# Kernel optimization log

Hardware: AMD Instinct MI355X
Metric: run time of the kernel (lower is better)

Reference implementation:

```python
import jax, jax.numpy as jnp
import numpy as np

EMBED_DIM = 1024
NUM_HEADS = 16
HEAD_DIM = EMBED_DIM // NUM_HEADS


def setup_inputs() -> dict:
    key = jax.random.key(0)
    k1, k2, k3, k4 = jax.random.split(key, 4)
    B, S, D = 2, 2048, EMBED_DIM
    x = jax.random.normal(k1, (B, S, D), dtype=jnp.float32)
    xpos = jax.random.randint(k2, (B, S), 0, 2048, dtype=jnp.int32)
    # torch nn.Linear weights: [out_features, in_features]; qkv_bias=False -> no qkv bias
    qkv_w = jax.random.normal(k3, (3 * D, D), dtype=jnp.float32) * (D ** -0.5)
    proj_w = jax.random.normal(k4, (D, D), dtype=jnp.float32) * (D ** -0.5)
    proj_b = jnp.zeros((D,), dtype=jnp.float32)
    return {"x": x, "xpos": xpos, "qkv_w": qkv_w, "proj_w": proj_w, "proj_b": proj_b}


def reference(x, xpos, qkv_w, proj_w, proj_b):
    # rope is None, dropout rates are 0, so xpos is unused and dropout is identity.
    B, S, D = x.shape
    H, hd = NUM_HEADS, D // NUM_HEADS
    scale = hd ** -0.5

    qkv = x @ qkv_w.T                                   # [B, S, 3D]
    qkv = qkv.reshape(B, S, 3, H, hd)
    qkv = jnp.transpose(qkv, (0, 3, 2, 1, 4))           # [B, H, 3, S, hd]
    q, k, v = qkv[:, :, 0], qkv[:, :, 1], qkv[:, :, 2]  # each [B, H, S, hd]

    scores = jnp.einsum("bhqd,bhkd->bhqk", q, k) * scale  # [B, H, S, S]
    probs = jax.nn.softmax(scores, axis=-1)
    out = jnp.einsum("bhqk,bhkd->bhqd", probs, v)         # [B, H, S, hd]

    out = jnp.transpose(out, (0, 2, 1, 3)).reshape(B, S, D)
    out = out @ proj_w.T + proj_b
    return out
```

## Files before the change

kernel.cpp:

```cpp
#include <hip/hip_runtime.h>


typedef __bf16 bf16_8 __attribute__((ext_vector_type(8)));
typedef __bf16 bf16_4 __attribute__((ext_vector_type(4)));
typedef __bf16 bf16_2 __attribute__((ext_vector_type(2)));
typedef float floatx2 __attribute__((ext_vector_type(2)));
typedef float floatx4 __attribute__((ext_vector_type(4)));
typedef float floatx16 __attribute__((ext_vector_type(16)));
typedef unsigned uintx4 __attribute__((ext_vector_type(4)));

#define MFMA16 __builtin_amdgcn_mfma_f32_16x16x32_bf16
#define MFMA32 __builtin_amdgcn_mfma_f32_32x32x16_bf16
#define CSCALE 0.1803368801111204f
#define EXP2R  __builtin_amdgcn_exp2f

__device__ __forceinline__ void gld16(const __bf16* g, __bf16* l) {
    __builtin_amdgcn_global_load_lds(
        (const __attribute__((address_space(1))) void*)g,
        (__attribute__((address_space(3))) void*)l, 16, 0, 0);
}

__device__ __forceinline__ unsigned cvtpk_bf16(float a, float b) {
    unsigned d;
    __asm__("v_cvt_pk_bf16_f32 %0, %1, %2" : "=v"(d) : "v"(a), "v"(b));
    return d;
}

__device__ __forceinline__ void pl32swap(unsigned& a, unsigned& b) {
    __asm__ __volatile__("v_permlane32_swap_b32 %0, %1" : "+v"(a), "+v"(b));
}

__global__ __launch_bounds__(256) void cvt_all(
    const float* __restrict__ x, const float* __restrict__ w1,
    const float* __restrict__ w2,
    __bf16* __restrict__ xb, __bf16* __restrict__ w1b, __bf16* __restrict__ w2b)
{
    const int i = blockIdx.x * 256 + threadIdx.x;
    const float* src; __bf16* dst; int off;
    if (i < (1 << 20))                  { src = x;  dst = xb;  off = i; }
    else if (i < (1 << 20) + 786432)    { src = w1; dst = w1b; off = i - (1 << 20); }
    else                                { src = w2; dst = w2b; off = i - (1 << 20) - 786432; }
    float4 v = ((const float4*)src)[off];
    bf16_4 o;
    o[0] = (__bf16)v.x; o[1] = (__bf16)v.y; o[2] = (__bf16)v.z; o[3] = (__bf16)v.w;
    ((bf16_4*)dst)[off] = o;
}

__global__ __launch_bounds__(512) void qkv_gemm(
    const __bf16* __restrict__ X, const __bf16* __restrict__ W,
    __bf16* __restrict__ q_ws, __bf16* __restrict__ k_ws, __bf16* __restrict__ vt_ws)
{
    __shared__ __align__(16) __bf16 S[2][2][128 * 32];

    const int tid = threadIdx.x, lane = tid & 63, wv = tid >> 6;
    const int quad = lane >> 4, l15 = lane & 15;
    const int wm = (wv >> 2) * 64, wn = (wv & 3) * 32;
    const int m0 = blockIdx.y * 128, n0 = blockIdx.x * 128;
    const int c = n0 >> 10;

    const __bf16* Abase;
    const __bf16* Bbase;
    if (c == 2) { Abase = X + (size_t)m0 * 1024; Bbase = W + (size_t)n0 * 1024; }
    else        { Abase = W + (size_t)n0 * 1024; Bbase = X + (size_t)m0 * 1024; }

    const int srow = tid >> 2, skc = tid & 3;
    const int ssw  = ((skc ^ (srow & 3)) * 8);

#define QKV_STAGE(buf, k0)                                                     \
    {                                                                          \
        gld16(Abase + srow * 1024 + (k0) + ssw, &S[buf][0][tid * 8]);          \
        gld16(Bbase + srow * 1024 + (k0) + ssw, &S[buf][1][tid * 8]);          \
    }

    floatx4 acc[4][2] = {};
    QKV_STAGE(0, 0)
    __syncthreads();

#pragma unroll 1
    for (int kk = 0; kk < 32; ++kk) {
        const int cur = kk & 1;
        if (kk < 31) QKV_STAGE(cur ^ 1, (kk + 1) * 32)

        const __bf16* As = S[cur][0];
        const __bf16* Bs = S[cur][1];
        bf16_8 af[4], bf[2];
#pragma unroll
        for (int mt = 0; mt < 4; ++mt) {
            int r = wm + mt * 16 + l15;
            af[mt] = *(const bf16_8*)&As[r * 32 + ((quad ^ (r & 3)) * 8)];
        }
#pragma unroll
        for (int nt = 0; nt < 2; ++nt) {
            int r = wn + nt * 16 + l15;
            bf[nt] = *(const bf16_8*)&Bs[r * 32 + ((quad ^ (r & 3)) * 8)];
        }
#pragma unroll
        for (int mt = 0; mt < 4; ++mt)
#pragma unroll
            for (int nt = 0; nt < 2; ++nt)
                acc[mt][nt] = MFMA16(af[mt], bf[nt], acc[mt][nt], 0, 0, 0);

        if (kk < 31) {
            __asm__ __volatile__("s_waitcnt vmcnt(0)" ::: "memory");
            __syncthreads();
        }
    }

    if (c == 2) {
#pragma unroll
        for (int mt = 0; mt < 4; ++mt) {
            const int mbase = m0 + wm + mt * 16 + quad * 4;
            const int b = mbase >> 11, s = mbase & 2047;
#pragma unroll
            for (int nt = 0; nt < 2; ++nt) {
                const int n = n0 + wn + nt * 16 + l15;
                const int h = (n >> 6) & 15, d = n & 63;
                bf16_4 pk;
#pragma unroll
                for (int r = 0; r < 4; ++r) pk[r] = (__bf16)acc[mt][nt][r];
                *(bf16_4*)&vt_ws[((size_t)(b * 16 + h) * 64 + d) * 2048 + s] = pk;
            }
        }
    } else {
        __bf16* dst = (c == 0) ? q_ws : k_ws;
        const float scale = (c == 1) ? CSCALE : 1.0f;
#pragma unroll
        for (int mt = 0; mt < 4; ++mt) {
            const int nn = n0 + wm + mt * 16 + quad * 4;
            const int h = (nn >> 6) & 15, d0 = nn & 63;
#pragma unroll
            for (int nt = 0; nt < 2; ++nt) {
                const int token = m0 + wn + nt * 16 + l15;
                const int b = token >> 11, skey = token & 2047;
                bf16_4 pk;
#pragma unroll
                for (int r = 0; r < 4; ++r) pk[r] = (__bf16)(acc[mt][nt][r] * scale);
                *(bf16_4*)&dst[((size_t)(b * 16 + h) * 2048 + skey) * 64 + d0] = pk;
            }
        }
    }
#undef QKV_STAGE
}

__global__ __launch_bounds__(512, 4) void attn_kernel(
    const __bf16* __restrict__ q_ws, const __bf16* __restrict__ k_ws,
    const __bf16* __restrict__ vt_ws, __bf16* __restrict__ attn_ws)
{
    __shared__ __align__(16) __bf16 Ks [2][2][64 * 64];
    __shared__ __align__(16) __bf16 Vts[2][2][64 * 64];

    const int tid = threadIdx.x, lane = tid & 63, w = tid >> 6;
    const int l31 = lane & 31, hi = lane >> 5;
    const int qtile = w & 3, keyhalf = w >> 2;
    const int htid = tid & 255;

    const int linear = blockIdx.x + (blockIdx.y << 4);
    const int r = linear >> 3;
    const int bh = ((linear & 7) << 2) + (r & 3);
    const int qt = r >> 2;
    const int q0 = qt * 128 + qtile * 32;

    const __bf16* __restrict__ qp  = q_ws  + (size_t)bh * (2048 * 64);
    const __bf16* __restrict__ kp  = k_ws  + (size_t)bh * (2048 * 64);
    const __bf16* __restrict__ vtp = vt_ws + (size_t)bh * (64 * 2048);
    const int koff = keyhalf * 1024;

    const int srow = htid >> 3, skc = htid & 7;
    const int sw   = (skc ^ (srow & 7)) * 8;
    const __bf16* kb0 = kp  + (size_t)(koff + srow) * 64 + sw;
    const __bf16* kb1 = kp  + (size_t)(koff + srow + 32) * 64 + sw;
    const __bf16* vb0 = vtp + (size_t)srow * 2048 + koff + sw;
    const __bf16* vb1 = vtp + (size_t)(srow + 32) * 2048 + koff + sw;
    const int ldsoff = htid * 8;

    bf16_8 qf[4];
    {
        const int qrow = q0 + l31;
#pragma unroll
        for (int s = 0; s < 4; ++s)
            qf[s] = *(const bf16_8*)&qp[qrow * 64 + s * 16 + hi * 8];
    }

    floatx16 oacc[2] = {};
    floatx2 ls2[4] = {};
    const floatx16 fzero = {};

    gld16(kb0, &Ks [keyhalf][0][ldsoff]);
    gld16(kb1, &Ks [keyhalf][0][ldsoff + 2048]);
    gld16(vb0, &Vts[keyhalf][0][ldsoff]);
    gld16(vb1, &Vts[keyhalf][0][ldsoff + 2048]);
    __syncthreads();

#pragma unroll 1
    for (int kt = 0; kt < 16; ++kt) {
        const int cur = kt & 1;
        if (kt < 15) {
            const int ko = (kt + 1) * 64;
            gld16(kb0 + ko * 64, &Ks [keyhalf][cur ^ 1][ldsoff]);
            gld16(kb1 + ko * 64, &Ks [keyhalf][cur ^ 1][ldsoff + 2048]);
            gld16(vb0 + ko,      &Vts[keyhalf][cur ^ 1][ldsoff]);
            gld16(vb1 + ko,      &Vts[keyhalf][cur ^ 1][ldsoff + 2048]);
        }
        const __bf16* Kb = Ks [keyhalf][cur];
        const __bf16* Vb = Vts[keyhalf][cur];

        floatx16 sacc[2];
        __builtin_amdgcn_s_setprio(1);
        {
            const int kc0 = hi;
            const int r0 = l31, r1 = 32 + l31;
            bf16_8 kf0 = *(const bf16_8*)&Kb[r0 * 64 + ((kc0 ^ (r0 & 7)) * 8)];
            bf16_8 kf1 = *(const bf16_8*)&Kb[r1 * 64 + ((kc0 ^ (r1 & 7)) * 8)];
            sacc[0] = MFMA32(kf0, qf[0], fzero, 0, 0, 0);
            sacc[1] = MFMA32(kf1, qf[0], fzero, 0, 0, 0);
        }
#pragma unroll
        for (int s = 1; s < 4; ++s) {
            const int kc = s * 2 + hi;
#pragma unroll
            for (int t = 0; t < 2; ++t) {
                const int row = t * 32 + l31;
                bf16_8 kf = *(const bf16_8*)&Kb[row * 64 + ((kc ^ (row & 7)) * 8)];
                sacc[t] = MFMA32(kf, qf[s], sacc[t], 0, 0, 0);
            }
        }
        __builtin_amdgcn_s_setprio(0);

#pragma unroll
        for (int s = 0; s < 4; ++s) {
            const int t = s >> 1, b2 = (s & 1) * 2;
            unsigned Dw[4];
#pragma unroll
            for (int jr = 0; jr < 2; ++jr)
#pragma unroll
                for (int e = 0; e < 2; ++e) {
                    const int j = b2 + jr;
                    float pa = EXP2R(sacc[t][j * 4 + e * 2]);
                    float pb = EXP2R(sacc[t][j * 4 + e * 2 + 1]);
                    floatx2 p2; p2[0] = pa; p2[1] = pb;
                    ls2[t * 2 + e] += p2;
                    Dw[jr * 2 + e] = cvtpk_bf16(pa, pb);
                }
            unsigned x0 = Dw[0], y0 = Dw[2];
            unsigned x1 = Dw[1], y1 = Dw[3];
            pl32swap(x0, y0);
            pl32swap(x1, y1);
            uintx4 uu; uu[0] = x0; uu[1] = x1; uu[2] = y0; uu[3] = y1;
            const bf16_8 pf = __builtin_bit_cast(bf16_8, uu);
            const int kc = s * 2 + hi;
            __builtin_amdgcn_s_setprio(1);
#pragma unroll
            for (int dt = 0; dt < 2; ++dt) {
                const int drow = dt * 32 + l31;
                bf16_8 vf = *(const bf16_8*)&Vb[drow * 64 + ((kc ^ (drow & 7)) * 8)];
                oacc[dt] = MFMA32(vf, pf, oacc[dt], 0, 0, 0);
            }
            __builtin_amdgcn_s_setprio(0);
        }

        if (kt < 15) {
            __asm__ __volatile__("s_waitcnt vmcnt(0)" ::: "memory");
            __syncthreads();
        }
    }

    const floatx2 lv = (ls2[0] + ls2[1]) + (ls2[2] + ls2[3]);
    const float lsum = lv[0] + lv[1];
    const float lw = lsum + __shfl_xor(lsum, 32, 64);

    __syncthreads();
    floatx4* comb  = (floatx4*)&Ks[0][0][0];
    float*   lcomb = (float*)&Vts[0][0][0];

    if (keyhalf == 1) {
#pragma unroll
        for (int dt = 0; dt < 2; ++dt)
#pragma unroll
            for (int g = 0; g < 4; ++g) {
                floatx4 v4;
#pragma unroll
                for (int r4 = 0; r4 < 4; ++r4) v4[r4] = oacc[dt][g * 4 + r4];
                comb[((qtile * 8 + dt * 4 + g) << 6) + lane] = v4;
            }
        lcomb[(qtile << 6) + lane] = lw;
    }
    __syncthreads();
    if (keyhalf == 0) {
        const int b = bh >> 4, h = bh & 15;
        const float inv_l = 1.0f / (lw + lcomb[(qtile << 6) + lane]);
        const int token = b * 2048 + q0 + l31;
#pragma unroll
        for (int dt = 0; dt < 2; ++dt)
#pragma unroll
            for (int g = 0; g < 4; ++g) {
                const floatx4 v2 = comb[((qtile * 8 + dt * 4 + g) << 6) + lane];
                bf16_4 ok;
#pragma unroll
                for (int r4 = 0; r4 < 4; ++r4)
                    ok[r4] = (__bf16)((oacc[dt][g * 4 + r4] + v2[r4]) * inv_l);
                *(bf16_4*)&attn_ws[(size_t)token * 1024 + h * 64 + dt * 32 + g * 8 + hi * 4] = ok;
            }
    }
}

__device__ __forceinline__ void proj_stage(
    const __bf16* __restrict__ A, const __bf16* __restrict__ Bp,
    int k0, __bf16* As, __bf16* Bs, int tid)
{
    const int srow = tid >> 3, skc = tid & 7;
    const int ssw  = (skc ^ (srow & 7)) * 8;
#pragma unroll
    for (int it = 0; it < 2; ++it) {
        const int row = srow + it * 64;
        gld16(A + row * 1024 + k0 + ssw, &As[(it * 512 + tid) * 8]);
    }
    gld16(Bp + srow * 1024 + k0 + ssw, &Bs[tid * 8]);
}

__global__ __launch_bounds__(512) void proj_gemm(
    const __bf16* __restrict__ Ain, const __bf16* __restrict__ W,
    const float* __restrict__ bias, float* __restrict__ out)
{
    __shared__ __align__(16) __bf16 As[2][128 * 64];
    __shared__ __align__(16) __bf16 Bs[2][64 * 64];
    floatx4 acc[2][2] = {};
    const int m0 = blockIdx.y * 128, n0 = blockIdx.x * 64;

    const int tid = threadIdx.x, lane = tid & 63, wv = tid >> 6;
    const int quad = lane >> 4, l15 = lane & 15;
    const int wm = (wv >> 1) * 32, wn = (wv & 1) * 32;

    const __bf16* A  = Ain + (size_t)m0 * 1024;
    const __bf16* Bp = W   + (size_t)n0 * 1024;

    proj_stage(A, Bp, 0, As[0], Bs[0], tid);
    __syncthreads();

#pragma unroll 1
    for (int kk = 0; kk < 16; ++kk) {
        const int cur = kk & 1;
        if (kk < 15)
            proj_stage(A, Bp, (kk + 1) * 64, As[cur ^ 1], Bs[cur ^ 1], tid);

        const __bf16* Ab = As[cur];
        const __bf16* Bb = Bs[cur];
#pragma unroll
        for (int ks = 0; ks < 2; ++ks) {
            bf16_8 af[2], bf[2];
#pragma unroll
            for (int mt = 0; mt < 2; ++mt) {
                int r = wm + mt * 16 + l15;
                af[mt] = *(const bf16_8*)&Ab[r * 64 + (((ks * 4 + quad) ^ (r & 7)) * 8)];
            }
#pragma unroll
            for (int nt = 0; nt < 2; ++nt) {
                int r = wn + nt * 16 + l15;
                bf[nt] = *(const bf16_8*)&Bb[r * 64 + (((ks * 4 + quad) ^ (r & 7)) * 8)];
            }
#pragma unroll
            for (int mt = 0; mt < 2; ++mt)
#pragma unroll
                for (int nt = 0; nt < 2; ++nt)
                    acc[mt][nt] = MFMA16(af[mt], bf[nt], acc[mt][nt], 0, 0, 0);
        }

        if (kk < 15) {
            __asm__ __volatile__("s_waitcnt vmcnt(0)" ::: "memory");
            __syncthreads();
        }
    }

    float bv[2];
#pragma unroll
    for (int nt = 0; nt < 2; ++nt) bv[nt] = bias[n0 + wn + nt * 16 + l15];

#pragma unroll
    for (int mt = 0; mt < 2; ++mt) {
        const int m = m0 + wm + mt * 16 + quad * 4;
#pragma unroll
        for (int nt = 0; nt < 2; ++nt) {
            const int n = n0 + wn + nt * 16 + l15;
#pragma unroll
            for (int r = 0; r < 4; ++r)
                out[(size_t)(m + r) * 1024 + n] = acc[mt][nt][r] + bv[nt];
        }
    }
}

extern "C" void kernel_launch(void* const* d_in, const int* in_sizes, int n_in,
                              void* d_out, int out_size, void* d_ws, size_t ws_size,
                              hipStream_t stream)
{
    const float* x      = (const float*)d_in[0];
    const float* qkv_w  = (const float*)d_in[2];
    const float* proj_w = (const float*)d_in[3];
    const float* proj_b = (const float*)d_in[4];
    float* out = (float*)d_out;

    const size_t SZ   = 4096 * 1024;
    const size_t WQKV = 3072 * 1024;
    const size_t WPRJ = 1024 * 1024;

    __bf16* xb      = (__bf16*)d_ws;
    __bf16* qkvwb   = xb + SZ;
    __bf16* projwb  = qkvwb + WQKV;
    __bf16* q_ws    = projwb + WPRJ;
    __bf16* k_ws    = q_ws + SZ;
    __bf16* vt_ws   = k_ws + SZ;
    __bf16* attn_ws = vt_ws + SZ;

    cvt_all<<<dim3(8192), 256, 0, stream>>>(x, qkv_w, proj_w, xb, qkvwb, projwb);
    qkv_gemm  <<<dim3(24, 32), 512, 0, stream>>>(xb, qkvwb, q_ws, k_ws, vt_ws);
    attn_kernel<<<dim3(16, 32), 512, 0, stream>>>(q_ws, k_ws, vt_ws, attn_ws);
    proj_gemm <<<dim3(16, 32), 512, 0, stream>>>(attn_ws, projwb, proj_b, out);
}
```

Measured before the change: 176.2 us.

## Fuse fp32-to-bf16 conversion into QKV and projection GEMM loaders

Measured after the change: 178.6 us. No clear change (+1.3%).

```diff
diff --git a/kernel.cpp b/kernel.cpp
--- a/kernel.cpp
+++ b/kernel.cpp
@@ -20,6 +20,13 @@
         (__attribute__((address_space(3))) void*)l, 16, 0, 0);
 }
 
+__device__ __forceinline__ bf16_8 cvt8(float4 a, float4 b) {
+    bf16_8 o;
+    o[0] = (__bf16)a.x; o[1] = (__bf16)a.y; o[2] = (__bf16)a.z; o[3] = (__bf16)a.w;
+    o[4] = (__bf16)b.x; o[5] = (__bf16)b.y; o[6] = (__bf16)b.z; o[7] = (__bf16)b.w;
+    return o;
+}
+
 __device__ __forceinline__ unsigned cvtpk_bf16(float a, float b) {
     unsigned d;
     __asm__("v_cvt_pk_bf16_f32 %0, %1, %2" : "=v"(d) : "v"(a), "v"(b));
@@ -30,24 +37,8 @@
     __asm__ __volatile__("v_permlane32_swap_b32 %0, %1" : "+v"(a), "+v"(b));
 }
 
-__global__ __launch_bounds__(256) void cvt_all(
-    const float* __restrict__ x, const float* __restrict__ w1,
-    const float* __restrict__ w2,
-    __bf16* __restrict__ xb, __bf16* __restrict__ w1b, __bf16* __restrict__ w2b)
-{
-    const int i = blockIdx.x * 256 + threadIdx.x;
-    const float* src; __bf16* dst; int off;
-    if (i < (1 << 20))                  { src = x;  dst = xb;  off = i; }
-    else if (i < (1 << 20) + 786432)    { src = w1; dst = w1b; off = i - (1 << 20); }
-    else                                { src = w2; dst = w2b; off = i - (1 << 20) - 786432; }
-    float4 v = ((const float4*)src)[off];
-    bf16_4 o;
-    o[0] = (__bf16)v.x; o[1] = (__bf16)v.y; o[2] = (__bf16)v.z; o[3] = (__bf16)v.w;
-    ((bf16_4*)dst)[off] = o;
-}
-
 __global__ __launch_bounds__(512) void qkv_gemm(
-    const __bf16* __restrict__ X, const __bf16* __restrict__ W,
+    const float* __restrict__ X, const float* __restrict__ W,
     __bf16* __restrict__ q_ws, __bf16* __restrict__ k_ws, __bf16* __restrict__ vt_ws)
 {
     __shared__ __align__(16) __bf16 S[2][2][128 * 32];
@@ -58,28 +49,37 @@
     const int m0 = blockIdx.y * 128, n0 = blockIdx.x * 128;
     const int c = n0 >> 10;
 
-    const __bf16* Abase;
-    const __bf16* Bbase;
+    const float* Abase;
+    const float* Bbase;
     if (c == 2) { Abase = X + (size_t)m0 * 1024; Bbase = W + (size_t)n0 * 1024; }
     else        { Abase = W + (size_t)n0 * 1024; Bbase = X + (size_t)m0 * 1024; }
 
     const int srow = tid >> 2, skc = tid & 3;
     const int ssw  = ((skc ^ (srow & 3)) * 8);
 
-#define QKV_STAGE(buf, k0)                                                     \
+    float4 a0, a1, b0, b1;
+
+#define QKV_LOAD(k0)                                                           \
     {                                                                          \
-        gld16(Abase + srow * 1024 + (k0) + ssw, &S[buf][0][tid * 8]);          \
-        gld16(Bbase + srow * 1024 + (k0) + ssw, &S[buf][1][tid * 8]);          \
+        const float4* ap = (const float4*)(Abase + srow * 1024 + (k0) + ssw);  \
+        const float4* bp = (const float4*)(Bbase + srow * 1024 + (k0) + ssw);  \
+        a0 = ap[0]; a1 = ap[1]; b0 = bp[0]; b1 = bp[1];                        \
+    }
+#define QKV_WRITE(buf)                                                         \
+    {                                                                          \
+        *(bf16_8*)&S[buf][0][tid * 8] = cvt8(a0, a1);                          \
+        *(bf16_8*)&S[buf][1][tid * 8] = cvt8(b0, b1);                          \
     }
 
     floatx4 acc[4][2] = {};
-    QKV_STAGE(0, 0)
+    QKV_LOAD(0)
+    QKV_WRITE(0)
     __syncthreads();
 
 #pragma unroll 1
     for (int kk = 0; kk < 32; ++kk) {
         const int cur = kk & 1;
-        if (kk < 31) QKV_STAGE(cur ^ 1, (kk + 1) * 32)
+        if (kk < 31) QKV_LOAD((kk + 1) * 32)
 
         const __bf16* As = S[cur][0];
         const __bf16* Bs = S[cur][1];
@@ -101,7 +101,7 @@
                 acc[mt][nt] = MFMA16(af[mt], bf[nt], acc[mt][nt], 0, 0, 0);
 
         if (kk < 31) {
-            __asm__ __volatile__("s_waitcnt vmcnt(0)" ::: "memory");
+            QKV_WRITE(cur ^ 1)
             __syncthreads();
         }
     }
@@ -139,7 +139,8 @@
             }
         }
     }
-#undef QKV_STAGE
+#undef QKV_LOAD
+#undef QKV_WRITE
 }
 
 __global__ __launch_bounds__(512, 4) void attn_kernel(
@@ -303,22 +304,8 @@
     }
 }
 
-__device__ __forceinline__ void proj_stage(
-    const __bf16* __restrict__ A, const __bf16* __restrict__ Bp,
-    int k0, __bf16* As, __bf16* Bs, int tid)
-{
-    const int srow = tid >> 3, skc = tid & 7;
-    const int ssw  = (skc ^ (srow & 7)) * 8;
-#pragma unroll
-    for (int it = 0; it < 2; ++it) {
-        const int row = srow + it * 64;
-        gld16(A + row * 1024 + k0 + ssw, &As[(it * 512 + tid) * 8]);
-    }
-    gld16(Bp + srow * 1024 + k0 + ssw, &Bs[tid * 8]);
-}
-
 __global__ __launch_bounds__(512) void proj_gemm(
-    const __bf16* __restrict__ Ain, const __bf16* __restrict__ W,
+    const __bf16* __restrict__ Ain, const float* __restrict__ W,
     const float* __restrict__ bias, float* __restrict__ out)
 {
     __shared__ __align__(16) __bf16 As[2][128 * 64];
@@ -331,16 +318,40 @@
     const int wm = (wv >> 1) * 32, wn = (wv & 1) * 32;
 
     const __bf16* A  = Ain + (size_t)m0 * 1024;
-    const __bf16* Bp = W   + (size_t)n0 * 1024;
-
-    proj_stage(A, Bp, 0, As[0], Bs[0], tid);
+    const float*  Bp = W   + (size_t)n0 * 1024;
+
+    const int srow = tid >> 3, skc = tid & 7;
+    const int ssw  = (skc ^ (srow & 7)) * 8;
+
+    float4 w0, w1;
+
+#define PROJ_STAGE_A(k0, buf)                                                  \
+    {                                                                          \
+        _Pragma("unroll")                                                      \
+        for (int it = 0; it < 2; ++it) {                      \
+            const int row = srow + it * 64;                                    \
+            gld16(A + row * 1024 + (k0) + ssw, &As[buf][(it * 512 + tid) * 8]);\
+        }                                                                      \
+    }
+#define PROJ_LOAD_B(k0)                                                        \
+    {                                                                          \
+        const float4* bp = (const float4*)(Bp + srow * 1024 + (k0) + ssw);     \
+        w0 = bp[0]; w1 = bp[1];                                                \
+    }
+
+    PROJ_STAGE_A(0, 0)
+    PROJ_LOAD_B(0)
+    *(bf16_8*)&Bs[0][tid * 8] = cvt8(w0, w1);
+    __asm__ __volatile__("s_waitcnt vmcnt(0)" ::: "memory");
     __syncthreads();
 
 #pragma unroll 1
     for (int kk = 0; kk < 16; ++kk) {
         const int cur = kk & 1;
-        if (kk < 15)
-            proj_stage(A, Bp, (kk + 1) * 64, As[cur ^ 1], Bs[cur ^ 1], tid);
+        if (kk < 15) {
+            PROJ_STAGE_A((kk + 1) * 64, cur ^ 1)
+            PROJ_LOAD_B((kk + 1) * 64)
+        }
 
         const __bf16* Ab = As[cur];
         const __bf16* Bb = Bs[cur];
@@ -365,6 +376,7 @@
         }
 
         if (kk < 15) {
+            *(bf16_8*)&Bs[cur ^ 1][tid * 8] = cvt8(w0, w1);
             __asm__ __volatile__("s_waitcnt vmcnt(0)" ::: "memory");
             __syncthreads();
         }
@@ -385,6 +397,8 @@
                 out[(size_t)(m + r) * 1024 + n] = acc[mt][nt][r] + bv[nt];
         }
     }
+#undef PROJ_STAGE_A
+#undef PROJ_LOAD_B
 }
 
 extern "C" void kernel_launch(void* const* d_in, const int* in_sizes, int n_in,
@@ -397,20 +411,14 @@
     const float* proj_b = (const float*)d_in[4];
     float* out = (float*)d_out;
 
-    const size_t SZ   = 4096 * 1024;
-    const size_t WQKV = 3072 * 1024;
-    const size_t WPRJ = 1024 * 1024;
-
-    __bf16* xb      = (__bf16*)d_ws;
-    __bf16* qkvwb   = xb + SZ;
-    __bf16* projwb  = qkvwb + WQKV;
-    __bf16* q_ws    = projwb + WPRJ;
+    const size_t SZ = 4096 * 1024;
+
+    __bf16* q_ws    = (__bf16*)d_ws;
     __bf16* k_ws    = q_ws + SZ;
     __bf16* vt_ws   = k_ws + SZ;
     __bf16* attn_ws = vt_ws + SZ;
 
-    cvt_all<<<dim3(8192), 256, 0, stream>>>(x, qkv_w, proj_w, xb, qkvwb, projwb);
-    qkv_gemm  <<<dim3(24, 32), 512, 0, stream>>>(xb, qkvwb, q_ws, k_ws, vt_ws);
+    qkv_gemm  <<<dim3(24, 32), 512, 0, stream>>>(x, qkv_w, q_ws, k_ws, vt_ws);
     attn_kernel<<<dim3(16, 32), 512, 0, stream>>>(q_ws, k_ws, vt_ws, attn_ws);
-    proj_gemm <<<dim3(16, 32), 512, 0, stream>>>(attn_ws, projwb, proj_b, out);
-}
+    proj_gemm <<<dim3(16, 32), 512, 0, stream>>>(attn_ws, proj_w, proj_b, out);
+}
```
